# Performance work log

Hardware: AMD Instinct MI355X
Metric: run time of the kernel (lower is better)

Reference implementation:

```python
import jax, jax.numpy as jnp
import numpy as np


def setup_inputs() -> dict:
    key = jax.random.key(0)
    ks = jax.random.split(key, 12)
    N, D, E = 50000, 64, 320000
    H0, H1, H2, OUT = 4 * D, 128, 128, 1  # edgemlp_size=[256,128,128], out_features=1
    h1 = jax.random.normal(ks[0], (N, D), dtype=jnp.float32)
    h2 = jax.random.normal(ks[1], (N, D), dtype=jnp.float32)
    src = jax.random.randint(ks[2], (E,), 0, N, dtype=jnp.int64)
    dst = jax.random.randint(ks[3], (E,), 0, N, dtype=jnp.int64)
    def lin_init(kw, kb, fan_in, fan_out):
        bound = 1.0 / np.sqrt(fan_in)
        W = jax.random.uniform(kw, (fan_out, fan_in), minval=-bound, maxval=bound, dtype=jnp.float32)
        b = jax.random.uniform(kb, (fan_out,), minval=-bound, maxval=bound, dtype=jnp.float32)
        return W, b
    W1, b1 = lin_init(ks[4], ks[5], H0, H1)
    W2, b2 = lin_init(ks[6], ks[7], H1, H2)
    W3, b3 = lin_init(ks[8], ks[9], H2, OUT)
    return {"h1": h1, "h2": h2, "src": src, "dst": dst,
            "W1": W1, "b1": b1, "W2": W2, "b2": b2, "W3": W3, "b3": b3}


def reference(h1, h2, src, dst, W1, b1, W2, b2, W3, b3):
    # Gather per-edge node features. NOTE: original code uses edges.src['h2']
    # for BOTH h2_u and h2_v (faithful to source), so h2 is gathered by src twice.
    h1_u = h1[src]            # [E, D]
    h1_v = h1[dst]            # [E, D]
    h2_u = h2[src]            # [E, D]
    h2_v = h2[src]            # [E, D]  (src, per original)
    h = jnp.concatenate([h1_u, h1_v, h2_u, h2_v], axis=1)  # [E, 4D]
    h = jax.nn.sigmoid(h @ W1.T + b1)
    h = jax.nn.sigmoid(h @ W2.T + b2)
    score = h @ W3.T + b3     # [E, out_features]
    return score
```

## Files before the change

kernel.cpp:

```cpp
#include <hip/hip_runtime.h>
#include <hip/hip_bf16.h>
#include <cstdint>


typedef __attribute__((ext_vector_type(8))) short bf16x8;
typedef __attribute__((ext_vector_type(4))) float f32x4;

__device__ __forceinline__ float sigmoid_fast(float x) {
    float e = __expf(-x);
    return __builtin_amdgcn_rcpf(1.0f + e);
}
__device__ __forceinline__ ushort f2bf_rne(float f) {
    uint32_t u = __float_as_uint(f);
    return (ushort)((u + 0x7fffu + ((u >> 16) & 1u)) >> 16);
}
__device__ __forceinline__ float bf2f_lo(uint32_t d) { return __uint_as_float(d << 16); }
__device__ __forceinline__ float bf2f_hi(uint32_t d) { return __uint_as_float(d & 0xffff0000u); }
__device__ __forceinline__ uint32_t packbf_rhu(float x, float y) {
    return ((__float_as_uint(x) + 0x8000u) >> 16) |
           ((__float_as_uint(y) + 0x8000u) & 0xffff0000u);
}

__global__ void prep_kernel(const float* __restrict__ W1, const float* __restrict__ W2,
                            ushort* __restrict__ WCF, ushort* __restrict__ WBF,
                            ushort* __restrict__ W2F) {
    int i = blockIdx.x * blockDim.x + threadIdx.x;
    if (i >= 16384) return;
    int j = i & 7, lf = (i >> 3) & 63, nt = (i >> 9) & 7, kk = i >> 12;
    int n = nt * 16 + (lf & 15);
    int kpos = kk * 32 + ((lf >> 4) << 3) + j;
    int ktrue = (kpos & ~31) | ((kpos >> 1) & 15) | ((kpos & 1) << 4);
    W2F[i] = f2bf_rne(W2[n * 128 + ktrue]);
    float v = (kpos < 64) ? W1[n * 256 + kpos]
                          : W1[n * 256 + 128 + (kpos - 64)] + W1[n * 256 + 192 + (kpos - 64)];
    WCF[i] = f2bf_rne(v);
    if (kk < 2) WBF[i] = f2bf_rne(W1[n * 256 + 64 + kpos]);
}

__global__ __launch_bounds__(256, 4) void node_kernel(
    const float* __restrict__ h1, const float* __restrict__ h2,
    const ushort* __restrict__ WCF, const ushort* __restrict__ WBF,
    const float* __restrict__ b1,
    uint32_t* __restrict__ Aout, uint32_t* __restrict__ Bout, int N)
{
    __shared__ __align__(16) ushort xt[64 * 136];
    const int tid = threadIdx.x, g = tid >> 6, ln = tid & 63;
    const int nl = ln & 15, q = ln >> 4;
    const int n0 = blockIdx.x * 64;

    bf16x8 fa[4][2], fb[2][2];
    #pragma unroll
    for (int kk = 0; kk < 4; ++kk)
        #pragma unroll
        for (int nt = 0; nt < 2; ++nt)
            fa[kk][nt] = *(const bf16x8*)(WCF + (((kk * 8 + g * 2 + nt) * 64 + ln) << 3));
    #pragma unroll
    for (int kk = 0; kk < 2; ++kk)
        #pragma unroll
        for (int nt = 0; nt < 2; ++nt)
            fb[kk][nt] = *(const bf16x8*)(WBF + (((kk * 8 + g * 2 + nt) * 64 + ln) << 3));
    const float b1c0 = b1[g * 32 + nl], b1c1 = b1[g * 32 + 16 + nl];

    #pragma unroll
    for (int i = 0; i < 8; ++i) {
        int local = i * 256 + tid;
        int node = local >> 5;
        int kq = (local & 31) * 4;
        float4 x = make_float4(0.f, 0.f, 0.f, 0.f);
        if (n0 + node < N)
            x = (kq < 64) ? *(const float4*)(h1 + (size_t)(n0 + node) * 64 + kq)
                          : *(const float4*)(h2 + (size_t)(n0 + node) * 64 + (kq - 64));
        uint32_t d0 = packbf_rhu(x.x, x.y), d1 = packbf_rhu(x.z, x.w);
        *(uint2*)&xt[node * 136 + kq] = make_uint2(d0, d1);
    }
    __syncthreads();

    #pragma unroll
    for (int m = 0; m < 4; ++m) {
        f32x4 accA[2], accB[2];
        #pragma unroll
        for (int r = 0; r < 4; ++r) { accA[0][r] = accA[1][r] = accB[0][r] = accB[1][r] = 0.f; }
        const ushort* arow = &xt[(m * 16 + nl) * 136 + (q << 3)];
        #pragma unroll
        for (int kk = 0; kk < 4; ++kk) {
            bf16x8 a = *(const bf16x8*)(arow + kk * 32);
            accA[0] = __builtin_amdgcn_mfma_f32_16x16x32_bf16(a, fa[kk][0], accA[0], 0, 0, 0);
            accA[1] = __builtin_amdgcn_mfma_f32_16x16x32_bf16(a, fa[kk][1], accA[1], 0, 0, 0);
            if (kk < 2) {
                accB[0] = __builtin_amdgcn_mfma_f32_16x16x32_bf16(a, fb[kk][0], accB[0], 0, 0, 0);
                accB[1] = __builtin_amdgcn_mfma_f32_16x16x32_bf16(a, fb[kk][1], accB[1], 0, 0, 0);
            }
        }
        #pragma unroll
        for (int r = 0; r < 4; ++r) {
            int node = n0 + m * 16 + q * 4 + r;
            if (node < N) {
                uint32_t da = packbf_rhu(accA[0][r] + b1c0, accA[1][r] + b1c1);
                uint32_t db = packbf_rhu(accB[0][r], accB[1][r]);
                Aout[(size_t)node * 64 + g * 16 + nl] = da;
                Bout[(size_t)node * 64 + g * 16 + nl] = db;
            }
        }
    }
}

__global__ __launch_bounds__(256, 4) void edge_kernel(
    const uint32_t* __restrict__ Am, const uint32_t* __restrict__ Bm,
    const int* __restrict__ src, const int* __restrict__ dst,
    const ushort* __restrict__ W2F, const float* __restrict__ b2,
    const float* __restrict__ W3, const float* __restrict__ b3,
    float* __restrict__ out, int E, int ntiles)
{
    __shared__ __align__(16) ushort hlds[64 * 136];
    __shared__ float part[4 * 64];
    const int tid = threadIdx.x, g = tid >> 6, ln = tid & 63;
    const int nl = ln & 15, q = ln >> 4;
    const int sub = ln >> 5, c = ln & 31;

    bf16x8 bfrag[8];
    #pragma unroll
    for (int kk = 0; kk < 4; ++kk)
        #pragma unroll
        for (int nt = 0; nt < 2; ++nt)
            bfrag[kk * 2 + nt] =
                *(const bf16x8*)(W2F + (((kk * 8 + g * 2 + nt) * 64 + ln) << 3));
    float b2c[2], w3c[2];
    #pragma unroll
    for (int nt = 0; nt < 2; ++nt) {
        int n = g * 32 + nt * 16 + nl;
        b2c[nt] = b2[n]; w3c[nt] = W3[n];
    }
    const float b3c = b3[0];

    for (int tile = blockIdx.x; tile < ntiles; tile += gridDim.x) {
        const int e0 = tile * 64;
        const int eb = e0 + g * 16;
        __syncthreads();

        int us = 0, vs = 0;
        if (ln < 16 && eb + ln < E) { us = src[eb + ln]; vs = dst[eb + ln]; }
        #pragma unroll
        for (int t = 0; t < 8; ++t) {
            int u0 = __builtin_amdgcn_readlane(us, 2 * t);
            int u1 = __builtin_amdgcn_readlane(us, 2 * t + 1);
            int v0 = __builtin_amdgcn_readlane(vs, 2 * t);
            int v1 = __builtin_amdgcn_readlane(vs, 2 * t + 1);
            int uu = sub ? u1 : u0;
            int vv = sub ? v1 : v0;
            uint2 av = *(const uint2*)(Am + (size_t)uu * 64 + 2 * c);
            uint2 bv = *(const uint2*)(Bm + (size_t)vv * 64 + 2 * c);
            float s0 = sigmoid_fast(bf2f_lo(av.x) + bf2f_lo(bv.x));
            float s1 = sigmoid_fast(bf2f_hi(av.x) + bf2f_hi(bv.x));
            float s2 = sigmoid_fast(bf2f_lo(av.y) + bf2f_lo(bv.y));
            float s3 = sigmoid_fast(bf2f_hi(av.y) + bf2f_hi(bv.y));
            uint32_t d0 = packbf_rhu(s0, s1), d1 = packbf_rhu(s2, s3);
            *(uint2*)&hlds[(g * 16 + 2 * t + sub) * 136 + c * 4] = make_uint2(d0, d1);
        }
        __syncthreads();

        #pragma unroll
        for (int m = 0; m < 4; ++m) {
            f32x4 acc[2];
            #pragma unroll
            for (int r = 0; r < 4; ++r) { acc[0][r] = 0.f; acc[1][r] = 0.f; }
            const ushort* arow = &hlds[(m * 16 + nl) * 136 + (q << 3)];
            #pragma unroll
            for (int kk = 0; kk < 4; ++kk) {
                bf16x8 a = *(const bf16x8*)(arow + kk * 32);
                acc[0] = __builtin_amdgcn_mfma_f32_16x16x32_bf16(a, bfrag[kk * 2],     acc[0], 0, 0, 0);
                acc[1] = __builtin_amdgcn_mfma_f32_16x16x32_bf16(a, bfrag[kk * 2 + 1], acc[1], 0, 0, 0);
            }
            float p[4] = {0.f, 0.f, 0.f, 0.f};
            #pragma unroll
            for (int nt = 0; nt < 2; ++nt)
                #pragma unroll
                for (int r = 0; r < 4; ++r)
                    p[r] = fmaf(w3c[nt], sigmoid_fast(acc[nt][r] + b2c[nt]), p[r]);
            #pragma unroll
            for (int r = 0; r < 4; ++r) {
                p[r] += __shfl_xor(p[r], 1, 16);
                p[r] += __shfl_xor(p[r], 2, 16);
                p[r] += __shfl_xor(p[r], 4, 16);
                p[r] += __shfl_xor(p[r], 8, 16);
            }
            if (nl == 0) {
                #pragma unroll
                for (int r = 0; r < 4; ++r)
                    part[g * 64 + m * 16 + q * 4 + r] = p[r];
            }
        }
        __syncthreads();
        if (tid < 64 && e0 + tid < E)
            out[e0 + tid] = (part[tid] + part[64 + tid])
                          + (part[128 + tid] + part[192 + tid]) + b3c;
    }
}

__global__ void naive_kernel(
    const float* __restrict__ h1, const float* __restrict__ h2,
    const int* __restrict__ src, const int* __restrict__ dst,
    const float* __restrict__ W1, const float* __restrict__ b1,
    const float* __restrict__ W2, const float* __restrict__ b2,
    const float* __restrict__ W3, const float* __restrict__ b3,
    float* __restrict__ out, int E, int N)
{
    int e = blockIdx.x * blockDim.x + threadIdx.x;
    if (e >= E) return;
    int u = src[e], v = dst[e];
    float h[128];
    for (int j = 0; j < 128; ++j) {
        float z = b1[j];
        const float* wj = W1 + j * 256;
        for (int k = 0; k < 64; ++k) {
            z += wj[k] * h1[(size_t)u * 64 + k]
               + wj[64 + k] * h1[(size_t)v * 64 + k]
               + (wj[128 + k] + wj[192 + k]) * h2[(size_t)u * 64 + k];
        }
        h[j] = 1.0f / (1.0f + __expf(-z));
    }
    float gg[128];
    for (int j = 0; j < 128; ++j) {
        float z = b2[j];
        for (int k = 0; k < 128; ++k) z = fmaf(W2[j * 128 + k], h[k], z);
        gg[j] = 1.0f / (1.0f + __expf(-z));
    }
    float s = b3[0];
    for (int j = 0; j < 128; ++j) s = fmaf(W3[j], gg[j], s);
    out[e] = s;
}

extern "C" void kernel_launch(void* const* d_in, const int* in_sizes, int n_in,
                              void* d_out, int out_size, void* d_ws, size_t ws_size,
                              hipStream_t stream) {
    const float* h1 = (const float*)d_in[0];
    const float* h2 = (const float*)d_in[1];
    const int*  src = (const int*)d_in[2];
    const int*  dst = (const int*)d_in[3];
    const float* W1 = (const float*)d_in[4];
    const float* b1 = (const float*)d_in[5];
    const float* W2 = (const float*)d_in[6];
    const float* b2 = (const float*)d_in[7];
    const float* W3 = (const float*)d_in[8];
    const float* b3 = (const float*)d_in[9];
    float* out = (float*)d_out;

    const int N = in_sizes[0] / 64;
    const int E = in_sizes[2];

    size_t offA   = 0;
    size_t offB   = offA + (size_t)N * 64;
    size_t offWCF = offB + (size_t)N * 64;
    size_t offWBF = offWCF + 8192;
    size_t offW2F = offWBF + 4096;
    size_t totalF = offW2F + 8192;

    if (ws_size < totalF * sizeof(float)) {
        naive_kernel<<<(E + 255) / 256, 256, 0, stream>>>(
            h1, h2, src, dst, W1, b1, W2, b2, W3, b3, out, E, N);
        return;
    }

    float* ws = (float*)d_ws;
    ushort* WCF = (ushort*)(ws + offWCF);
    ushort* WBF = (ushort*)(ws + offWBF);
    ushort* W2F = (ushort*)(ws + offW2F);

    prep_kernel<<<64, 256, 0, stream>>>(W1, W2, WCF, WBF, W2F);
    node_kernel<<<(N + 63) / 64, 256, 0, stream>>>(
        h1, h2, WCF, WBF, b1, (uint32_t*)(ws + offA), (uint32_t*)(ws + offB), N);
    const int ntiles = (E + 63) / 64;
    edge_kernel<<<1000, 256, 0, stream>>>(
        (const uint32_t*)(ws + offA), (const uint32_t*)(ws + offB), src, dst,
        W2F, b2, W3, b3, out, E, ntiles);
}
```

Measured before the change: 137.2 us.

## Software-pipeline edge gathers into registers with double-buffered LDS

The edge kernel now prefetches the next tile's src/dst indices and A/B row gathers into registers while the current tile is processed. It double-buffers the hidden-activation LDS tile and the partial-sum array so each iteration needs one barrier instead of two, and the output write of a tile is deferred to the next iteration. Gathers become 16-byte loads with four lanes per edge instead of 8-byte loads with 32 lanes per edge. The grid grows from 1000 to 2500 blocks, and the node kernel skips bounds checks for full blocks. The cost is more registers and twice the LDS per block, which can lower occupancy.

```diff
diff --git a/kernel.cpp b/kernel.cpp
--- a/kernel.cpp
+++ b/kernel.cpp
@@ -47,6 +47,7 @@
     const int tid = threadIdx.x, g = tid >> 6, ln = tid & 63;
     const int nl = ln & 15, q = ln >> 4;
     const int n0 = blockIdx.x * 64;
+    const bool full = (n0 + 64 <= N);
 
     bf16x8 fa[4][2], fb[2][2];
     #pragma unroll
@@ -67,7 +68,7 @@
         int node = local >> 5;
         int kq = (local & 31) * 4;
         float4 x = make_float4(0.f, 0.f, 0.f, 0.f);
-        if (n0 + node < N)
+        if (full || n0 + node < N)
             x = (kq < 64) ? *(const float4*)(h1 + (size_t)(n0 + node) * 64 + kq)
                           : *(const float4*)(h2 + (size_t)(n0 + node) * 64 + (kq - 64));
         uint32_t d0 = packbf_rhu(x.x, x.y), d1 = packbf_rhu(x.z, x.w);
@@ -94,11 +95,9 @@
         #pragma unroll
         for (int r = 0; r < 4; ++r) {
             int node = n0 + m * 16 + q * 4 + r;
-            if (node < N) {
-                uint32_t da = packbf_rhu(accA[0][r] + b1c0, accA[1][r] + b1c1);
-                uint32_t db = packbf_rhu(accB[0][r], accB[1][r]);
-                Aout[(size_t)node * 64 + g * 16 + nl] = da;
-                Bout[(size_t)node * 64 + g * 16 + nl] = db;
+            if (full || node < N) {
+                Aout[(size_t)node * 64 + g * 16 + nl] = packbf_rhu(accA[0][r] + b1c0, accA[1][r] + b1c1);
+                Bout[(size_t)node * 64 + g * 16 + nl] = packbf_rhu(accB[0][r], accB[1][r]);
             }
         }
     }
@@ -111,11 +110,12 @@
     const float* __restrict__ W3, const float* __restrict__ b3,
     float* __restrict__ out, int E, int ntiles)
 {
-    __shared__ __align__(16) ushort hlds[64 * 136];
-    __shared__ float part[4 * 64];
+    __shared__ __align__(16) ushort hlds[2][64 * 136];
+    __shared__ float part[2][256];
     const int tid = threadIdx.x, g = tid >> 6, ln = tid & 63;
     const int nl = ln & 15, q = ln >> 4;
-    const int sub = ln >> 5, c = ln & 31;
+    const int el = g * 16 + (ln >> 2);
+    const int p  = ln & 3;
 
     bf16x8 bfrag[8];
     #pragma unroll
@@ -132,67 +132,97 @@
     }
     const float b3c = b3[0];
 
-    for (int tile = blockIdx.x; tile < ntiles; tile += gridDim.x) {
-        const int e0 = tile * 64;
-        const int eb = e0 + g * 16;
+    uint4 ga[4], gb[4];
+    int t = blockIdx.x;
+    if (t < ntiles) {
+        int eb = t * 64 + g * 16, us = 0, vs = 0;
+        if (ln < 16 && eb + ln < E) { us = src[eb + ln]; vs = dst[eb + ln]; }
+        int uu = __shfl(us, ln >> 2), vv = __shfl(vs, ln >> 2);
+        const uint32_t* ap = Am + (size_t)uu * 64 + p * 4;
+        const uint32_t* bp = Bm + (size_t)vv * 64 + p * 4;
+        #pragma unroll
+        for (int r = 0; r < 4; ++r) {
+            ga[r] = *(const uint4*)(ap + r * 16);
+            gb[r] = *(const uint4*)(bp + r * 16);
+        }
+    }
+    int buf = 0, prev = -1;
+    for (; t < ntiles; t += gridDim.x) {
+        #pragma unroll
+        for (int r = 0; r < 4; ++r) {
+            uint32_t sa[4] = {ga[r].x, ga[r].y, ga[r].z, ga[r].w};
+            uint32_t sb[4] = {gb[r].x, gb[r].y, gb[r].z, gb[r].w};
+            uint32_t da[4];
+            #pragma unroll
+            for (int d = 0; d < 4; ++d) {
+                float zl = bf2f_lo(sa[d]) + bf2f_lo(sb[d]);
+                float zh = bf2f_hi(sa[d]) + bf2f_hi(sb[d]);
+                da[d] = packbf_rhu(sigmoid_fast(zl), sigmoid_fast(zh));
+            }
+            *(uint4*)&hlds[buf][el * 136 + r * 32 + p * 8] =
+                make_uint4(da[0], da[1], da[2], da[3]);
+        }
+        int tn = t + gridDim.x;
+        if (tn < ntiles) {
+            int eb = tn * 64 + g * 16, us = 0, vs = 0;
+            if (ln < 16 && eb + ln < E) { us = src[eb + ln]; vs = dst[eb + ln]; }
+            int uu = __shfl(us, ln >> 2), vv = __shfl(vs, ln >> 2);
+            const uint32_t* ap = Am + (size_t)uu * 64 + p * 4;
+            const uint32_t* bp = Bm + (size_t)vv * 64 + p * 4;
+            #pragma unroll
+            for (int r = 0; r < 4; ++r) {
+                ga[r] = *(const uint4*)(ap + r * 16);
+                gb[r] = *(const uint4*)(bp + r * 16);
+            }
+        }
         __syncthreads();
 
-        int us = 0, vs = 0;
-        if (ln < 16 && eb + ln < E) { us = src[eb + ln]; vs = dst[eb + ln]; }
-        #pragma unroll
-        for (int t = 0; t < 8; ++t) {
-            int u0 = __builtin_amdgcn_readlane(us, 2 * t);
-            int u1 = __builtin_amdgcn_readlane(us, 2 * t + 1);
-            int v0 = __builtin_amdgcn_readlane(vs, 2 * t);
-            int v1 = __builtin_amdgcn_readlane(vs, 2 * t + 1);
-            int uu = sub ? u1 : u0;
-            int vv = sub ? v1 : v0;
-            uint2 av = *(const uint2*)(Am + (size_t)uu * 64 + 2 * c);
-            uint2 bv = *(const uint2*)(Bm + (size_t)vv * 64 + 2 * c);
-            float s0 = sigmoid_fast(bf2f_lo(av.x) + bf2f_lo(bv.x));
-            float s1 = sigmoid_fast(bf2f_hi(av.x) + bf2f_hi(bv.x));
-            float s2 = sigmoid_fast(bf2f_lo(av.y) + bf2f_lo(bv.y));
-            float s3 = sigmoid_fast(bf2f_hi(av.y) + bf2f_hi(bv.y));
-            uint32_t d0 = packbf_rhu(s0, s1), d1 = packbf_rhu(s2, s3);
-            *(uint2*)&hlds[(g * 16 + 2 * t + sub) * 136 + c * 4] = make_uint2(d0, d1);
-        }
-        __syncthreads();
+        if (prev >= 0 && tid < 64) {
+            int e = prev * 64 + tid;
+            if (e < E)
+                out[e] = (part[buf ^ 1][tid] + part[buf ^ 1][64 + tid])
+                       + (part[buf ^ 1][128 + tid] + part[buf ^ 1][192 + tid]) + b3c;
+        }
 
         #pragma unroll
         for (int m = 0; m < 4; ++m) {
             f32x4 acc[2];
             #pragma unroll
             for (int r = 0; r < 4; ++r) { acc[0][r] = 0.f; acc[1][r] = 0.f; }
-            const ushort* arow = &hlds[(m * 16 + nl) * 136 + (q << 3)];
+            const ushort* arow = &hlds[buf][(m * 16 + nl) * 136 + (q << 3)];
             #pragma unroll
             for (int kk = 0; kk < 4; ++kk) {
                 bf16x8 a = *(const bf16x8*)(arow + kk * 32);
                 acc[0] = __builtin_amdgcn_mfma_f32_16x16x32_bf16(a, bfrag[kk * 2],     acc[0], 0, 0, 0);
                 acc[1] = __builtin_amdgcn_mfma_f32_16x16x32_bf16(a, bfrag[kk * 2 + 1], acc[1], 0, 0, 0);
             }
-            float p[4] = {0.f, 0.f, 0.f, 0.f};
+            float pr[4] = {0.f, 0.f, 0.f, 0.f};
             #pragma unroll
             for (int nt = 0; nt < 2; ++nt)
                 #pragma unroll
                 for (int r = 0; r < 4; ++r)
-                    p[r] = fmaf(w3c[nt], sigmoid_fast(acc[nt][r] + b2c[nt]), p[r]);
+                    pr[r] = fmaf(w3c[nt], sigmoid_fast(acc[nt][r] + b2c[nt]), pr[r]);
             #pragma unroll
             for (int r = 0; r < 4; ++r) {
-                p[r] += __shfl_xor(p[r], 1, 16);
-                p[r] += __shfl_xor(p[r], 2, 16);
-                p[r] += __shfl_xor(p[r], 4, 16);
-                p[r] += __shfl_xor(p[r], 8, 16);
+                pr[r] += __shfl_xor(pr[r], 1, 16);
+                pr[r] += __shfl_xor(pr[r], 2, 16);
+                pr[r] += __shfl_xor(pr[r], 4, 16);
+                pr[r] += __shfl_xor(pr[r], 8, 16);
             }
             if (nl == 0) {
                 #pragma unroll
                 for (int r = 0; r < 4; ++r)
-                    part[g * 64 + m * 16 + q * 4 + r] = p[r];
-            }
-        }
-        __syncthreads();
-        if (tid < 64 && e0 + tid < E)
-            out[e0 + tid] = (part[tid] + part[64 + tid])
-                          + (part[128 + tid] + part[192 + tid]) + b3c;
+                    part[buf][g * 64 + m * 16 + q * 4 + r] = pr[r];
+            }
+        }
+        prev = t; buf ^= 1;
+    }
+    __syncthreads();
+    if (prev >= 0 && tid < 64) {
+        int e = prev * 64 + tid;
+        if (e < E)
+            out[e] = (part[buf ^ 1][tid] + part[buf ^ 1][64 + tid])
+                   + (part[buf ^ 1][128 + tid] + part[buf ^ 1][192 + tid]) + b3c;
     }
 }
 
@@ -269,7 +299,7 @@
     node_kernel<<<(N + 63) / 64, 256, 0, stream>>>(
         h1, h2, WCF, WBF, b1, (uint32_t*)(ws + offA), (uint32_t*)(ws + offB), N);
     const int ntiles = (E + 63) / 64;
-    edge_kernel<<<1000, 256, 0, stream>>>(
+    edge_kernel<<<2500, 256, 0, stream>>>(
         (const uint32_t*)(ws + offA), (const uint32_t*)(ws + offB), src, dst,
         W2F, b2, W3, b3, out, E, ntiles);
 }
```

New measurement: 130.8 us. 1.05x faster.
